# Optimization experiments

Measured on AMD Instinct MI355X. Metric: run time of the kernel, lower is better.

## Reference

```python
import jax, jax.numpy as jnp
import numpy as np

B, H, W, C = 16, 64, 64, 512
C2 = C // 2
LN_EPS = 1e-3  # Keras LayerNormalization default epsilon


def setup_inputs() -> dict:
    key = jax.random.key(0)
    ks = jax.random.split(key, 8)
    s = 0.02
    return {
        "x": jax.random.normal(ks[0], (B, H, W, C), dtype=jnp.float32),
        "ch_wv_w": jax.random.normal(ks[1], (C, C2), dtype=jnp.float32) * s,
        "ch_wv_b": jnp.zeros((C2,), jnp.float32),
        "ch_wq_w": jax.random.normal(ks[2], (C, 1), dtype=jnp.float32) * s,
        "ch_wq_b": jnp.zeros((1,), jnp.float32),
        "ch_wz_w": jax.random.normal(ks[3], (C2, C), dtype=jnp.float32) * s,
        "ch_wz_b": jnp.zeros((C,), jnp.float32),
        "ln_gamma": jnp.ones((C,), jnp.float32),
        "ln_beta": jnp.zeros((C,), jnp.float32),
        "sp_wv_w": jax.random.normal(ks[4], (C, C2), dtype=jnp.float32) * s,
        "sp_wv_b": jnp.zeros((C2,), jnp.float32),
        "sp_wq_w": jax.random.normal(ks[5], (C, C2), dtype=jnp.float32) * s,
        "sp_wq_b": jnp.zeros((C2,), jnp.float32),
    }


def reference(x, ch_wv_w, ch_wv_b, ch_wq_w, ch_wq_b, ch_wz_w, ch_wz_b,
              ln_gamma, ln_beta, sp_wv_w, sp_wv_b, sp_wq_w, sp_wq_b):
    b, h, w, c = x.shape
    n = h * w
    c2 = c // 2

    # ---- channel-only branch ----
    # 1x1 convs are pointwise GEMMs over the channel dim
    ch_wv = jnp.einsum('bhwc,cd->bhwd', x, ch_wv_w) + ch_wv_b      # (B,H,W,C/2)
    ch_wq = jnp.einsum('bhwc,co->bhwo', x, ch_wq_w) + ch_wq_b      # (B,H,W,1)
    ch_wv = ch_wv.reshape(b, n, c2)                                # (B,N,C/2)
    ch_wq = jax.nn.softmax(ch_wq.reshape(b, n, 1), axis=1)         # softmax over N
    ch_wz = jnp.einsum('bnd,bno->bd', ch_wv, ch_wq)                # (B,C/2)
    ch_wz = jnp.einsum('bd,dc->bc', ch_wz, ch_wz_w) + ch_wz_b      # (B,C)

    # LayerNorm over axes [1,2,3] of (B,1,1,C) == normalize over C
    mean = jnp.mean(ch_wz, axis=-1, keepdims=True)
    var = jnp.var(ch_wz, axis=-1, keepdims=True)
    ch_wz = (ch_wz - mean) * jax.lax.rsqrt(var + LN_EPS) * ln_gamma + ln_beta
    channel_weight = jax.nn.sigmoid(ch_wz)[:, None, None, :]       # (B,1,1,C)
    channel_out = channel_weight * x                               # (B,H,W,C)

    # ---- spatial-only branch ----
    sp_wv = jnp.einsum('bhwc,cd->bhwd', channel_out, sp_wv_w) + sp_wv_b  # (B,H,W,C/2)
    sp_wq = jnp.einsum('bhwc,cd->bhwd', channel_out, sp_wq_w) + sp_wq_b  # (B,H,W,C/2)
    sp_wq = jnp.mean(sp_wq, axis=(1, 2))                           # GAP -> (B,C/2)
    sp_wq = jax.nn.softmax(sp_wq, axis=-1)                         # softmax over C/2
    sp_wv = sp_wv.reshape(b, n, c2)                                # (B,N,C/2)
    sp_wz = jnp.einsum('bd,bnd->bn', sp_wq, sp_wv)                 # (B,N)
    spatial_weight = jax.nn.sigmoid(sp_wz).reshape(b, h, w, 1)     # (B,H,W,1)
    return spatial_weight * channel_out
```

## Files before the change

kernel.cpp:

```cpp
#include <hip/hip_runtime.h>
#include <math.h>

#define BB 16
#define NN 4096
#define CC 512
#define C2 256
#define CHUNKS 32
#define RPC (NN/CHUNKS)
#define NW (CC*C2)

typedef float  f4v __attribute__((ext_vector_type(4)));
typedef unsigned short ushort;
typedef unsigned int   uint;

__device__ __forceinline__ float sigmoidf_(float z){ return 1.0f/(1.0f + __expf(-z)); }
__device__ __forceinline__ float dot8_(float4 a0, float4 a1, float4 b0, float4 b1){
    return a0.x*b0.x + a0.y*b0.y + a0.z*b0.z + a0.w*b0.w
         + a1.x*b1.x + a1.y*b1.y + a1.z*b1.z + a1.w*b1.w;
}
__device__ __forceinline__ float bf2f(ushort u){ return __uint_as_float(((uint)u) << 16); }
__device__ __forceinline__ ushort f2bf(float f){
    uint u = __float_as_uint(f);
    return (ushort)((u + 0x7FFFu + ((u >> 16) & 1u)) >> 16);
}
__device__ __forceinline__ float2 bfpair(uint v){
    return make_float2(__uint_as_float(v << 16), __uint_as_float(v & 0xFFFF0000u));
}

__global__ __launch_bounds__(256) void k_stats(const float* __restrict__ x,
        const float* __restrict__ wq,
        const float* __restrict__ Wv, const float* __restrict__ Wz,
        const float* __restrict__ Wq2, const float* __restrict__ Wv2,
        float* __restrict__ part_w, float* __restrict__ part_g,
        float* __restrict__ part_d, ushort* __restrict__ wbf)
{
    const int t = threadIdx.x, lane = t & 63, wv = t >> 6;

    if (blockIdx.x >= BB*CHUNKS) {
        const int idx = blockIdx.x - BB*CHUNKS;
        const int mat = idx >> 4;
        const float* src = (mat == 0) ? Wv : (mat == 1) ? Wz : (mat == 2) ? Wq2 : Wv2;
        const int boff = (idx & 15) * 8192;
        ushort* dst = wbf + (long)mat*NW + boff;
        const float* s = src + boff;
        #pragma unroll 8
        for (int e = 0; e < 32; ++e)
            dst[t + e*256] = f2bf(s[t + e*256]);
        return;
    }

    const int b = blockIdx.x / CHUNKS;
    const int k = blockIdx.x % CHUNKS;
    __shared__ float rw[4][CC];
    __shared__ float rg[4][CC];
    __shared__ float rd[4];
    const long base = ((long)b*NN + (long)k*RPC) * CC;

    float4 w0 = *(const float4*)(wq + lane*4);
    float4 w1 = *(const float4*)(wq + 256 + lane*4);
    float4 aw0={0,0,0,0}, aw1={0,0,0,0}, ag0={0,0,0,0}, ag1={0,0,0,0};
    float den = 0.f;

    for (int i = 0; i < RPC/4; ++i) {
        const int r = wv*(RPC/4) + i;
        const float* xr = x + base + (long)r*CC;
        float4 a0 = *(const float4*)(xr + lane*4);
        float4 a1 = *(const float4*)(xr + 256 + lane*4);
        float d = dot8_(a0, a1, w0, w1);
        #pragma unroll
        for (int off = 32; off; off >>= 1) d += __shfl_xor(d, off);
        const float e = __expf(d);
        den += e;
        aw0.x = fmaf(e,a0.x,aw0.x); aw0.y = fmaf(e,a0.y,aw0.y);
        aw0.z = fmaf(e,a0.z,aw0.z); aw0.w = fmaf(e,a0.w,aw0.w);
        aw1.x = fmaf(e,a1.x,aw1.x); aw1.y = fmaf(e,a1.y,aw1.y);
        aw1.z = fmaf(e,a1.z,aw1.z); aw1.w = fmaf(e,a1.w,aw1.w);
        ag0.x += a0.x; ag0.y += a0.y; ag0.z += a0.z; ag0.w += a0.w;
        ag1.x += a1.x; ag1.y += a1.y; ag1.z += a1.z; ag1.w += a1.w;
    }
    *(float4*)&rw[wv][lane*4]     = aw0;
    *(float4*)&rw[wv][256+lane*4] = aw1;
    *(float4*)&rg[wv][lane*4]     = ag0;
    *(float4*)&rg[wv][256+lane*4] = ag1;
    if (lane == 0) rd[wv] = den;
    __syncthreads();

    const long o = (long)(b*CHUNKS + k)*CC;
    part_w[o + t]       = rw[0][t]+rw[1][t]+rw[2][t]+rw[3][t];
    part_w[o + t + 256] = rw[0][t+256]+rw[1][t+256]+rw[2][t+256]+rw[3][t+256];
    part_g[o + t]       = rg[0][t]+rg[1][t]+rg[2][t]+rg[3][t];
    part_g[o + t + 256] = rg[0][t+256]+rg[1][t+256]+rg[2][t+256]+rg[3][t+256];
    if (t == 0) part_d[b*CHUNKS + k] = rd[0]+rd[1]+rd[2]+rd[3];
}

__global__ __launch_bounds__(512) void k_chain(
    const float* __restrict__ part_w, const float* __restrict__ part_g,
    const float* __restrict__ part_d,
    const ushort* __restrict__ wbf,
    const float* __restrict__ bv,  const float* __restrict__ bz,
    const float* __restrict__ lng, const float* __restrict__ lnb,
    const float* __restrict__ bq,  const float* __restrict__ bv2,
    float* __restrict__ cw, float* __restrict__ veff, float* __restrict__ constb)
{
    const int b = blockIdx.x, t = threadIdx.x, lane = t & 63, w = t >> 6;
    const ushort* Wvb  = wbf;
    const ushort* Wzb  = wbf + NW;
    const ushort* Wqb  = wbf + 2*NW;
    const ushort* Wv2b = wbf + 3*NW;
    __shared__ float s_a[CC];
    __shared__ float s_b[CC];
    __shared__ float s_c[CC];
    __shared__ float s_m[C2];
    __shared__ float s_r[16];

    {
        const float* pwp = part_w + (long)b*CHUNKS*CC + t;
        const float* pgp = part_g + (long)b*CHUNKS*CC + t;
        float pw = 0.f, pg = 0.f;
        #pragma unroll 8
        for (int k = 0; k < CHUNKS; ++k) {
            pw += __builtin_nontemporal_load(pwp + (long)k*CC);
            pg += __builtin_nontemporal_load(pgp + (long)k*CC);
        }
        const float* pd = part_d + b*CHUNKS;
        float den = 0.f;
        #pragma unroll 8
        for (int k = 0; k < CHUNKS; ++k) den += pd[k];
        s_a[t] = pw / den;
        s_b[t] = pg;
    }
    __syncthreads();

    {
        const int d = t & 255, ch = t >> 8;
        const ushort* wp = Wvb + (long)(ch*256)*C2 + d;
        const float* xp = s_a + ch*256;
        float a0=0,a1=0,a2=0,a3=0;
        #pragma unroll 8
        for (int c = 0; c < 256; c += 4) {
            a0 = fmaf(xp[c+0], bf2f(wp[(long)(c+0)*C2]), a0);
            a1 = fmaf(xp[c+1], bf2f(wp[(long)(c+1)*C2]), a1);
            a2 = fmaf(xp[c+2], bf2f(wp[(long)(c+2)*C2]), a2);
            a3 = fmaf(xp[c+3], bf2f(wp[(long)(c+3)*C2]), a3);
        }
        s_c[t] = (a0+a1)+(a2+a3);
    }
    __syncthreads();
    if (t < 256) s_m[t] = s_c[t] + s_c[t+256] + bv[t];
    __syncthreads();

    float zt;
    {
        const ushort* wp = Wzb + t;
        float a0=0,a1=0,a2=0,a3=0;
        #pragma unroll 8
        for (int d = 0; d < 256; d += 4) {
            a0 = fmaf(s_m[d+0], bf2f(wp[(long)(d+0)*CC]), a0);
            a1 = fmaf(s_m[d+1], bf2f(wp[(long)(d+1)*CC]), a1);
            a2 = fmaf(s_m[d+2], bf2f(wp[(long)(d+2)*CC]), a2);
            a3 = fmaf(s_m[d+3], bf2f(wp[(long)(d+3)*CC]), a3);
        }
        zt = (a0+a1)+(a2+a3) + bz[t];
    }

    {
        float sum = zt, sq = zt*zt;
        #pragma unroll
        for (int off = 32; off; off >>= 1) { sum += __shfl_xor(sum, off); sq += __shfl_xor(sq, off); }
        if (lane == 0) { s_r[w] = sum; s_r[8+w] = sq; }
        __syncthreads();
        sum = 0.f; sq = 0.f;
        #pragma unroll
        for (int i = 0; i < 8; ++i) { sum += s_r[i]; sq += s_r[8+i]; }
        const float mean = sum * (1.f/CC);
        const float var  = sq  * (1.f/CC) - mean*mean;
        const float rstd = rsqrtf(var + 1e-3f);
        const float cwt = sigmoidf_((zt - mean)*rstd*lng[t] + lnb[t]);
        cw[b*CC + t] = cwt;
        __syncthreads();
        s_c[t] = cwt;
        s_a[t] = cwt * s_b[t] * (1.f/NN);
    }
    __syncthreads();

    {
        const int d = t & 255, ch = t >> 8;
        const ushort* wp = Wqb + (long)(ch*256)*C2 + d;
        const float* xp = s_a + ch*256;
        float a0=0,a1=0,a2=0,a3=0;
        #pragma unroll 8
        for (int c = 0; c < 256; c += 4) {
            a0 = fmaf(xp[c+0], bf2f(wp[(long)(c+0)*C2]), a0);
            a1 = fmaf(xp[c+1], bf2f(wp[(long)(c+1)*C2]), a1);
            a2 = fmaf(xp[c+2], bf2f(wp[(long)(c+2)*C2]), a2);
            a3 = fmaf(xp[c+3], bf2f(wp[(long)(c+3)*C2]), a3);
        }
        s_b[t] = (a0+a1)+(a2+a3);
    }
    __syncthreads();

    float qv = 0.f;
    if (t < 256) qv = s_b[t] + s_b[t+256] + bq[t];
    {
        float mx = (t < 256) ? qv : -3.4e38f;
        #pragma unroll
        for (int off = 32; off; off >>= 1) mx = fmaxf(mx, __shfl_xor(mx, off));
        if (lane == 0) s_r[w] = mx;
        __syncthreads();
        mx = s_r[0];
        #pragma unroll
        for (int i = 1; i < 8; ++i) mx = fmaxf(mx, s_r[i]);
        float e = (t < 256) ? __expf(qv - mx) : 0.f;
        float se = e;
        #pragma unroll
        for (int off = 32; off; off >>= 1) se += __shfl_xor(se, off);
        __syncthreads();
        if (lane == 0) s_r[8+w] = se;
        __syncthreads();
        se = 0.f;
        #pragma unroll
        for (int i = 0; i < 8; ++i) se += s_r[8+i];
        const float qn = e / se;
        float cb = (t < 256) ? qn * bv2[t] : 0.f;
        #pragma unroll
        for (int off = 32; off; off >>= 1) cb += __shfl_xor(cb, off);
        if (lane == 0) s_r[w] = cb;
        __syncthreads();
        if (t < 256) s_b[t] = qn;
        if (t == 0) {
            float c_ = 0.f;
            #pragma unroll
            for (int i = 0; i < 8; ++i) c_ += s_r[i];
            constb[b] = c_;
        }
    }
    __syncthreads();

    {
        const int sub = lane & 15;
        float4 q0 = *(const float4*)(s_b + sub*16 + 0);
        float4 q1 = *(const float4*)(s_b + sub*16 + 4);
        float4 q2 = *(const float4*)(s_b + sub*16 + 8);
        float4 q3 = *(const float4*)(s_b + sub*16 + 12);
        for (int it = 0; it < 16; ++it) {
            const int c = (it*8 + w)*4 + (lane >> 4);
            const uint4* wr = (const uint4*)(Wv2b + (long)c*C2) + sub*2;
            uint4 u0 = wr[0], u1 = wr[1];
            float2 p;
            float d = 0.f;
            p = bfpair(u0.x); d += p.x*q0.x + p.y*q0.y;
            p = bfpair(u0.y); d += p.x*q0.z + p.y*q0.w;
            p = bfpair(u0.z); d += p.x*q1.x + p.y*q1.y;
            p = bfpair(u0.w); d += p.x*q1.z + p.y*q1.w;
            p = bfpair(u1.x); d += p.x*q2.x + p.y*q2.y;
            p = bfpair(u1.y); d += p.x*q2.z + p.y*q2.w;
            p = bfpair(u1.z); d += p.x*q3.x + p.y*q3.y;
            p = bfpair(u1.w); d += p.x*q3.z + p.y*q3.w;
            #pragma unroll
            for (int off = 8; off; off >>= 1) d += __shfl_xor(d, off);
            if (sub == 0) veff[b*CC + c] = s_c[c] * d;
        }
    }
}

__global__ __launch_bounds__(256) void k_final(const float* __restrict__ x,
        const float* __restrict__ cw, const float* __restrict__ veff,
        const float* __restrict__ constb, float* __restrict__ out)
{
    const int lane = threadIdx.x & 63;
    const int wv   = threadIdx.x >> 6;
    const long row = (long)blockIdx.x * 4 + wv;
    const int b = (int)(row >> 12);
    const float* xr = x + row * CC;
    float4 a0 = *(const float4*)(xr + lane*4);
    float4 a1 = *(const float4*)(xr + 256 + lane*4);
    const float* vb = veff + b*CC;
    float4 v0 = *(const float4*)(vb + lane*4);
    float4 v1 = *(const float4*)(vb + 256 + lane*4);
    float d = dot8_(a0, a1, v0, v1);
    #pragma unroll
    for (int off = 32; off; off >>= 1) d += __shfl_xor(d, off);
    const float sw = sigmoidf_(d + constb[b]);
    const float* cb = cw + b*CC;
    float4 c0 = *(const float4*)(cb + lane*4);
    float4 c1 = *(const float4*)(cb + 256 + lane*4);
    f4v o0 = { sw*c0.x*a0.x, sw*c0.y*a0.y, sw*c0.z*a0.z, sw*c0.w*a0.w };
    f4v o1 = { sw*c1.x*a1.x, sw*c1.y*a1.y, sw*c1.z*a1.z, sw*c1.w*a1.w };
    __builtin_nontemporal_store(o0, (f4v*)(out + row*CC + lane*4));
    __builtin_nontemporal_store(o1, (f4v*)(out + row*CC + 256 + lane*4));
}

extern "C" void kernel_launch(void* const* d_in, const int* in_sizes, int n_in,
                              void* d_out, int out_size, void* d_ws, size_t ws_size,
                              hipStream_t stream)
{
    const float* x       = (const float*)d_in[0];
    const float* ch_wv_w = (const float*)d_in[1];
    const float* ch_wv_b = (const float*)d_in[2];
    const float* ch_wq_w = (const float*)d_in[3];
    const float* ch_wz_w = (const float*)d_in[5];
    const float* ch_wz_b = (const float*)d_in[6];
    const float* ln_g    = (const float*)d_in[7];
    const float* ln_b    = (const float*)d_in[8];
    const float* sp_wv_w = (const float*)d_in[9];
    const float* sp_wv_b = (const float*)d_in[10];
    const float* sp_wq_w = (const float*)d_in[11];
    const float* sp_wq_b = (const float*)d_in[12];
    float* out = (float*)d_out;

    float* ws = (float*)d_ws;
    float* part_w  = ws;
    float* part_g  = part_w + BB*CHUNKS*CC;
    float* part_d  = part_g + BB*CHUNKS*CC;
    float* cw      = part_d + BB*CHUNKS;
    float* veff    = cw + BB*CC;
    float* constb  = veff + BB*CC;
    ushort* wbf    = (ushort*)(constb + BB);

    k_stats<<<BB*CHUNKS + 64, 256, 0, stream>>>(x, ch_wq_w,
                                                ch_wv_w, ch_wz_w, sp_wq_w, sp_wv_w,
                                                part_w, part_g, part_d, wbf);
    k_chain<<<BB,  512, 0, stream>>>(part_w, part_g, part_d, wbf,
                                     ch_wv_b, ch_wz_b, ln_g, ln_b, sp_wq_b, sp_wv_b,
                                     cw, veff, constb);
    k_final<<<BB*NN/4, 256, 0, stream>>>(x, cw, veff, constb, out);
}
```

Before: 95.35 us.

## Double chunk count, process two rows per wave, and pair bf16 weight loads

Doubles the stats-pass chunk count for more blocks, and unrolls the stats and final kernels to handle two rows per wave, so two shuffle reductions and more loads are in flight at once. The k_chain matvecs now load bf16 weights as packed pairs with 32-bit loads and split the reduction dimension across more threads, combining partials in a new shared buffer. The costs are more partial sums for k_chain to read (CHUNKS doubled) and higher register use per thread.

Result: no change. 94.97 us (-0.4%).

```diff
diff --git a/kernel.cpp b/kernel.cpp
--- a/kernel.cpp
+++ b/kernel.cpp
@@ -5,7 +5,7 @@
 #define NN 4096
 #define CC 512
 #define C2 256
-#define CHUNKS 32
+#define CHUNKS 64
 #define RPC (NN/CHUNKS)
 #define NW (CC*C2)
 
@@ -18,7 +18,6 @@
     return a0.x*b0.x + a0.y*b0.y + a0.z*b0.z + a0.w*b0.w
          + a1.x*b1.x + a1.y*b1.y + a1.z*b1.z + a1.w*b1.w;
 }
-__device__ __forceinline__ float bf2f(ushort u){ return __uint_as_float(((uint)u) << 16); }
 __device__ __forceinline__ ushort f2bf(float f){
     uint u = __float_as_uint(f);
     return (ushort)((u + 0x7FFFu + ((u >> 16) & 1u)) >> 16);
@@ -61,22 +60,30 @@
     float4 aw0={0,0,0,0}, aw1={0,0,0,0}, ag0={0,0,0,0}, ag1={0,0,0,0};
     float den = 0.f;
 
-    for (int i = 0; i < RPC/4; ++i) {
-        const int r = wv*(RPC/4) + i;
-        const float* xr = x + base + (long)r*CC;
-        float4 a0 = *(const float4*)(xr + lane*4);
-        float4 a1 = *(const float4*)(xr + 256 + lane*4);
-        float d = dot8_(a0, a1, w0, w1);
-        #pragma unroll
-        for (int off = 32; off; off >>= 1) d += __shfl_xor(d, off);
-        const float e = __expf(d);
-        den += e;
-        aw0.x = fmaf(e,a0.x,aw0.x); aw0.y = fmaf(e,a0.y,aw0.y);
-        aw0.z = fmaf(e,a0.z,aw0.z); aw0.w = fmaf(e,a0.w,aw0.w);
-        aw1.x = fmaf(e,a1.x,aw1.x); aw1.y = fmaf(e,a1.y,aw1.y);
-        aw1.z = fmaf(e,a1.z,aw1.z); aw1.w = fmaf(e,a1.w,aw1.w);
-        ag0.x += a0.x; ag0.y += a0.y; ag0.z += a0.z; ag0.w += a0.w;
-        ag1.x += a1.x; ag1.y += a1.y; ag1.z += a1.z; ag1.w += a1.w;
+    for (int i = 0; i < RPC/8; ++i) {
+        const int r0 = wv*(RPC/4) + 2*i;
+        const float* xr0 = x + base + (long)r0*CC;
+        const float* xr1 = xr0 + CC;
+        float4 a0 = *(const float4*)(xr0 + lane*4);
+        float4 a1 = *(const float4*)(xr0 + 256 + lane*4);
+        float4 b0 = *(const float4*)(xr1 + lane*4);
+        float4 b1 = *(const float4*)(xr1 + 256 + lane*4);
+        float da = dot8_(a0, a1, w0, w1);
+        float db = dot8_(b0, b1, w0, w1);
+        #pragma unroll
+        for (int off = 32; off; off >>= 1) {
+            da += __shfl_xor(da, off);
+            db += __shfl_xor(db, off);
+        }
+        const float ea = __expf(da);
+        const float eb = __expf(db);
+        den += ea + eb;
+        aw0.x = fmaf(ea,a0.x,fmaf(eb,b0.x,aw0.x)); aw0.y = fmaf(ea,a0.y,fmaf(eb,b0.y,aw0.y));
+        aw0.z = fmaf(ea,a0.z,fmaf(eb,b0.z,aw0.z)); aw0.w = fmaf(ea,a0.w,fmaf(eb,b0.w,aw0.w));
+        aw1.x = fmaf(ea,a1.x,fmaf(eb,b1.x,aw1.x)); aw1.y = fmaf(ea,a1.y,fmaf(eb,b1.y,aw1.y));
+        aw1.z = fmaf(ea,a1.z,fmaf(eb,b1.z,aw1.z)); aw1.w = fmaf(ea,a1.w,fmaf(eb,b1.w,aw1.w));
+        ag0.x += a0.x+b0.x; ag0.y += a0.y+b0.y; ag0.z += a0.z+b0.z; ag0.w += a0.w+b0.w;
+        ag1.x += a1.x+b1.x; ag1.y += a1.y+b1.y; ag1.z += a1.z+b1.z; ag1.w += a1.w+b1.w;
     }
     *(float4*)&rw[wv][lane*4]     = aw0;
     *(float4*)&rw[wv][256+lane*4] = aw1;
@@ -111,6 +118,7 @@
     __shared__ float s_b[CC];
     __shared__ float s_c[CC];
     __shared__ float s_m[C2];
+    __shared__ float s_g1[1024];
     __shared__ float s_r[16];
 
     {
@@ -132,36 +140,43 @@
     __syncthreads();
 
     {
-        const int d = t & 255, ch = t >> 8;
-        const ushort* wp = Wvb + (long)(ch*256)*C2 + d;
-        const float* xp = s_a + ch*256;
-        float a0=0,a1=0,a2=0,a3=0;
-        #pragma unroll 8
-        for (int c = 0; c < 256; c += 4) {
-            a0 = fmaf(xp[c+0], bf2f(wp[(long)(c+0)*C2]), a0);
-            a1 = fmaf(xp[c+1], bf2f(wp[(long)(c+1)*C2]), a1);
-            a2 = fmaf(xp[c+2], bf2f(wp[(long)(c+2)*C2]), a2);
-            a3 = fmaf(xp[c+3], bf2f(wp[(long)(c+3)*C2]), a3);
-        }
-        s_c[t] = (a0+a1)+(a2+a3);
-    }
-    __syncthreads();
-    if (t < 256) s_m[t] = s_c[t] + s_c[t+256] + bv[t];
-    __syncthreads();
-
-    float zt;
-    {
-        const ushort* wp = Wzb + t;
-        float a0=0,a1=0,a2=0,a3=0;
-        #pragma unroll 8
-        for (int d = 0; d < 256; d += 4) {
-            a0 = fmaf(s_m[d+0], bf2f(wp[(long)(d+0)*CC]), a0);
-            a1 = fmaf(s_m[d+1], bf2f(wp[(long)(d+1)*CC]), a1);
-            a2 = fmaf(s_m[d+2], bf2f(wp[(long)(d+2)*CC]), a2);
-            a3 = fmaf(s_m[d+3], bf2f(wp[(long)(d+3)*CC]), a3);
-        }
-        zt = (a0+a1)+(a2+a3) + bz[t];
-    }
+        const int pr = t & 127, cq = t >> 7;
+        const ushort* wp = Wvb + (long)(cq*128)*C2 + 2*pr;
+        const float* xp = s_a + cq*128;
+        float ax=0, ay=0, bx=0, by=0;
+        #pragma unroll 8
+        for (int c = 0; c < 128; c += 2) {
+            uint u0 = *(const uint*)(wp + (long)(c  )*C2);
+            uint u1 = *(const uint*)(wp + (long)(c+1)*C2);
+            float2 p0 = bfpair(u0), p1 = bfpair(u1);
+            ax = fmaf(xp[c],   p0.x, ax); ay = fmaf(xp[c],   p0.y, ay);
+            bx = fmaf(xp[c+1], p1.x, bx); by = fmaf(xp[c+1], p1.y, by);
+        }
+        s_g1[cq*256 + pr*2]     = ax + bx;
+        s_g1[cq*256 + pr*2 + 1] = ay + by;
+    }
+    __syncthreads();
+    if (t < 256) s_m[t] = s_g1[t] + s_g1[256+t] + s_g1[512+t] + s_g1[768+t] + bv[t];
+    __syncthreads();
+
+    {
+        const int cp = t & 255, dh = t >> 8;
+        const ushort* wp = Wzb + (long)(dh*128)*CC + 2*cp;
+        const float* mp = s_m + dh*128;
+        float ax=0, ay=0, bx=0, by=0;
+        #pragma unroll 8
+        for (int d = 0; d < 128; d += 2) {
+            uint u0 = *(const uint*)(wp + (long)(d  )*CC);
+            uint u1 = *(const uint*)(wp + (long)(d+1)*CC);
+            float2 p0 = bfpair(u0), p1 = bfpair(u1);
+            ax = fmaf(mp[d],   p0.x, ax); ay = fmaf(mp[d],   p0.y, ay);
+            bx = fmaf(mp[d+1], p1.x, bx); by = fmaf(mp[d+1], p1.y, by);
+        }
+        s_g1[dh*512 + cp*2]     = ax + bx;
+        s_g1[dh*512 + cp*2 + 1] = ay + by;
+    }
+    __syncthreads();
+    float zt = s_g1[t] + s_g1[512 + t] + bz[t];
 
     {
         float sum = zt, sq = zt*zt;
@@ -184,23 +199,25 @@
     __syncthreads();
 
     {
-        const int d = t & 255, ch = t >> 8;
-        const ushort* wp = Wqb + (long)(ch*256)*C2 + d;
-        const float* xp = s_a + ch*256;
-        float a0=0,a1=0,a2=0,a3=0;
-        #pragma unroll 8
-        for (int c = 0; c < 256; c += 4) {
-            a0 = fmaf(xp[c+0], bf2f(wp[(long)(c+0)*C2]), a0);
-            a1 = fmaf(xp[c+1], bf2f(wp[(long)(c+1)*C2]), a1);
-            a2 = fmaf(xp[c+2], bf2f(wp[(long)(c+2)*C2]), a2);
-            a3 = fmaf(xp[c+3], bf2f(wp[(long)(c+3)*C2]), a3);
-        }
-        s_b[t] = (a0+a1)+(a2+a3);
+        const int pr = t & 127, cq = t >> 7;
+        const ushort* wp = Wqb + (long)(cq*128)*C2 + 2*pr;
+        const float* xp = s_a + cq*128;
+        float ax=0, ay=0, bx=0, by=0;
+        #pragma unroll 8
+        for (int c = 0; c < 128; c += 2) {
+            uint u0 = *(const uint*)(wp + (long)(c  )*C2);
+            uint u1 = *(const uint*)(wp + (long)(c+1)*C2);
+            float2 p0 = bfpair(u0), p1 = bfpair(u1);
+            ax = fmaf(xp[c],   p0.x, ax); ay = fmaf(xp[c],   p0.y, ay);
+            bx = fmaf(xp[c+1], p1.x, bx); by = fmaf(xp[c+1], p1.y, by);
+        }
+        s_g1[cq*256 + pr*2]     = ax + bx;
+        s_g1[cq*256 + pr*2 + 1] = ay + by;
     }
     __syncthreads();
 
     float qv = 0.f;
-    if (t < 256) qv = s_b[t] + s_b[t+256] + bq[t];
+    if (t < 256) qv = s_g1[t] + s_g1[256+t] + s_g1[512+t] + s_g1[768+t] + bq[t];
     {
         float mx = (t < 256) ? qv : -3.4e38f;
         #pragma unroll
@@ -269,25 +286,37 @@
 {
     const int lane = threadIdx.x & 63;
     const int wv   = threadIdx.x >> 6;
-    const long row = (long)blockIdx.x * 4 + wv;
-    const int b = (int)(row >> 12);
-    const float* xr = x + row * CC;
-    float4 a0 = *(const float4*)(xr + lane*4);
-    float4 a1 = *(const float4*)(xr + 256 + lane*4);
+    const long row0 = (long)blockIdx.x * 8 + wv*2;
+    const int b = (int)(row0 >> 12);
     const float* vb = veff + b*CC;
     float4 v0 = *(const float4*)(vb + lane*4);
     float4 v1 = *(const float4*)(vb + 256 + lane*4);
-    float d = dot8_(a0, a1, v0, v1);
-    #pragma unroll
-    for (int off = 32; off; off >>= 1) d += __shfl_xor(d, off);
-    const float sw = sigmoidf_(d + constb[b]);
     const float* cb = cw + b*CC;
     float4 c0 = *(const float4*)(cb + lane*4);
     float4 c1 = *(const float4*)(cb + 256 + lane*4);
-    f4v o0 = { sw*c0.x*a0.x, sw*c0.y*a0.y, sw*c0.z*a0.z, sw*c0.w*a0.w };
-    f4v o1 = { sw*c1.x*a1.x, sw*c1.y*a1.y, sw*c1.z*a1.z, sw*c1.w*a1.w };
-    __builtin_nontemporal_store(o0, (f4v*)(out + row*CC + lane*4));
-    __builtin_nontemporal_store(o1, (f4v*)(out + row*CC + 256 + lane*4));
+    const float* xr0 = x + row0 * CC;
+    float4 a0 = *(const float4*)(xr0 + lane*4);
+    float4 a1 = *(const float4*)(xr0 + 256 + lane*4);
+    float4 b0 = *(const float4*)(xr0 + CC + lane*4);
+    float4 b1 = *(const float4*)(xr0 + CC + 256 + lane*4);
+    float d0 = dot8_(a0, a1, v0, v1);
+    float d1 = dot8_(b0, b1, v0, v1);
+    #pragma unroll
+    for (int off = 32; off; off >>= 1) {
+        d0 += __shfl_xor(d0, off);
+        d1 += __shfl_xor(d1, off);
+    }
+    const float cbb = constb[b];
+    const float sw0 = sigmoidf_(d0 + cbb);
+    const float sw1 = sigmoidf_(d1 + cbb);
+    f4v o0 = { sw0*c0.x*a0.x, sw0*c0.y*a0.y, sw0*c0.z*a0.z, sw0*c0.w*a0.w };
+    f4v o1 = { sw0*c1.x*a1.x, sw0*c1.y*a1.y, sw0*c1.z*a1.z, sw0*c1.w*a1.w };
+    f4v o2 = { sw1*c0.x*b0.x, sw1*c0.y*b0.y, sw1*c0.z*b0.z, sw1*c0.w*b0.w };
+    f4v o3 = { sw1*c1.x*b1.x, sw1*c1.y*b1.y, sw1*c1.z*b1.z, sw1*c1.w*b1.w };
+    __builtin_nontemporal_store(o0, (f4v*)(out + row0*CC + lane*4));
+    __builtin_nontemporal_store(o1, (f4v*)(out + row0*CC + 256 + lane*4));
+    __builtin_nontemporal_store(o2, (f4v*)(out + row0*CC + CC + lane*4));
+    __builtin_nontemporal_store(o3, (f4v*)(out + row0*CC + CC + 256 + lane*4));
 }
 
 extern "C" void kernel_launch(void* const* d_in, const int* in_sizes, int n_in,
@@ -323,5 +352,5 @@
     k_chain<<<BB,  512, 0, stream>>>(part_w, part_g, part_d, wbf,
                                      ch_wv_b, ch_wz_b, ln_g, ln_b, sp_wq_b, sp_wv_b,
                                      cw, veff, constb);
-    k_final<<<BB*NN/4, 256, 0, stream>>>(x, cw, veff, constb, out);
-}
+    k_final<<<BB*NN/8, 256, 0, stream>>>(x, cw, veff, constb, out);
+}
```
